# Optimization experiments

Measured on AMD Instinct MI355X. Metric: run time of the kernel, lower is better.

Reference implementation:

```python
import jax, jax.numpy as jnp
import numpy as np

N = 100_000   # nodes
E = 1_280_000 # edges
F_IN = 64
HID = 64

def setup_inputs() -> dict:
    key = jax.random.key(0)
    ks = jax.random.split(key, 5)
    x = jax.random.normal(ks[0], (N, F_IN), dtype=jnp.float32)
    edge_index = jax.random.randint(ks[1], (2, E), 0, N, dtype=jnp.int32)
    edge_weight = jax.random.uniform(ks[2], (E,), dtype=jnp.float32)
    s1 = 1.0 / np.sqrt(F_IN)
    W1 = jax.random.uniform(ks[3], (F_IN, HID), minval=-s1, maxval=s1, dtype=jnp.float32)
    b1 = jnp.zeros((HID,), jnp.float32)
    s2 = 1.0 / np.sqrt(HID)
    W2 = jax.random.uniform(ks[4], (HID, 1), minval=-s2, maxval=s2, dtype=jnp.float32)
    b2 = jnp.zeros((1,), jnp.float32)
    return {"x": x, "edge_index": edge_index, "edge_weight": edge_weight,
            "W1": W1, "b1": b1, "W2": W2, "b2": b2}


def reference(x, edge_index, edge_weight, W1, b1, W2, b2):
    # eval mode: edge dropout and feature dropout are identity.
    # GCNConv with add_self_loops=True: A_hat = A + I, D_hat^-1/2 A_hat D_hat^-1/2.
    row, col = edge_index[0], edge_index[1]
    sl = jnp.arange(N, dtype=row.dtype)
    row = jnp.concatenate([row, sl])
    col = jnp.concatenate([col, sl])
    w = jnp.concatenate([edge_weight, jnp.ones((N,), edge_weight.dtype)])
    # symmetric normalization (shared by both conv layers)
    deg = jax.ops.segment_sum(w, col, num_segments=N)          # [N]
    dinv = jnp.where(deg > 0, jax.lax.rsqrt(deg), 0.0)
    norm = dinv[row] * w * dinv[col]                           # [E+N]

    def gcn(h):  # h: [N, d] already linearly transformed
        msg = h[row] * norm[:, None]                           # gather + scale
        return jax.ops.segment_sum(msg, col, num_segments=N)   # scatter-add

    h = gcn(x @ W1) + b1          # conv1
    h = jax.nn.relu(h)            # relu (dropout = identity in eval)
    out = gcn(h @ W2) + b2        # conv2 -> [N, 1]
    return out
```

## Files before the change

### kernel.cpp

```cpp
#include <hip/hip_runtime.h>
#include <hip/hip_fp16.h>

#define CNT_SHIFT 26
#define DEG_MASK  ((1u << CNT_SHIFT) - 1)
#define DEG_SCALE 1048576.0f
#define CAP 8192
#define GSTRIDE 16

__device__ __forceinline__ unsigned short f_to_h16(float f) {
    return __half_as_ushort(__float2half(f));
}
__device__ __forceinline__ float h16_to_f(unsigned short u) {
    return __half2float(__ushort_as_half(u));
}
__device__ __forceinline__ unsigned long long mkrec(int r, int c, float wv) {
    return (unsigned long long)r | ((unsigned long long)(c & 511) << 17)
         | ((unsigned long long)f_to_h16(wv) << 26);
}

__global__ __launch_bounds__(256) void k_scatter_gemm(
        const int4* __restrict__ row4, const int4* __restrict__ col4, const float4* __restrict__ w4,
        const int* __restrict__ row, const int* __restrict__ col, const float* __restrict__ w,
        unsigned* __restrict__ gcur, unsigned long long* __restrict__ binrec,
        const float* __restrict__ x, const float* __restrict__ W1,
        char* __restrict__ h1q, float* __restrict__ scales,
        int E4, int rem, int nBlkE, int nGemm, int n, int nbkt) {
    __shared__ int h[256];
    __shared__ float xs[4][512];
    int blk = blockIdx.x, t = threadIdx.x;
    if (blk < nBlkE) {
        h[t] = 0;
        __syncthreads();
        int base = blk * 1024;
#pragma unroll
        for (int k = 0; k < 4; ++k) {
            int g = base + k * 256 + t;
            if (g < E4) {
                int4 c = col4[g];
                atomicAdd(&h[c.x >> 9], 1);
                atomicAdd(&h[c.y >> 9], 1);
                atomicAdd(&h[c.z >> 9], 1);
                atomicAdd(&h[c.w >> 9], 1);
            }
        }
        if (blk == 0 && t < rem) atomicAdd(&h[col[4 * E4 + t] >> 9], 1);
        __syncthreads();
        if (t < nbkt) {
            int bb = t + (blk % nbkt);
            bb -= (bb >= nbkt) ? nbkt : 0;
            int cnt = h[bb];
            int runbase = 0;
            if (cnt > 0) runbase = (int)atomicAdd(&gcur[(size_t)bb * GSTRIDE], (unsigned)cnt);
            h[bb] = bb * CAP + runbase;
        }
        __syncthreads();
#pragma unroll
        for (int k = 0; k < 4; ++k) {
            int g = base + k * 256 + t;
            if (g < E4) {
                int4   r = row4[g];
                int4   c = col4[g];
                float4 v = w4[g];
                { int pos = atomicAdd(&h[c.x >> 9], 1); binrec[pos] = mkrec(r.x, c.x, v.x); }
                { int pos = atomicAdd(&h[c.y >> 9], 1); binrec[pos] = mkrec(r.y, c.y, v.y); }
                { int pos = atomicAdd(&h[c.z >> 9], 1); binrec[pos] = mkrec(r.z, c.z, v.z); }
                { int pos = atomicAdd(&h[c.w >> 9], 1); binrec[pos] = mkrec(r.w, c.w, v.w); }
            }
        }
        if (blk == 0 && t < rem) {
            int e = 4 * E4 + t;
            int c = col[e];
            int pos = atomicAdd(&h[c >> 9], 1);
            binrec[pos] = mkrec(row[e], c, w[e]);
        }
    } else {
        int b = blk - nBlkE;
        int lane = t & 63, wave = t >> 6;
        float wr[64];
#pragma unroll
        for (int k = 0; k < 64; ++k) wr[k] = W1[k * 64 + lane];
        const int stride = nGemm * 32;
        for (int base = b * 32 + wave * 8; base < n; base += stride) {
            if (base + 8 <= n) {
                const float4* xsrc = (const float4*)(x + (size_t)base * 64);
                *(float4*)&xs[wave][4 * lane]       = xsrc[lane];
                *(float4*)&xs[wave][256 + 4 * lane] = xsrc[lane + 64];
            } else {
                const float* xf = x + (size_t)base * 64;
                int valid = (n - base) * 64;
                float4 a0, a1;
                int f0 = 4 * lane, f1 = 256 + 4 * lane;
                a0.x = (f0 + 0 < valid) ? xf[f0 + 0] : 0.f;
                a0.y = (f0 + 1 < valid) ? xf[f0 + 1] : 0.f;
                a0.z = (f0 + 2 < valid) ? xf[f0 + 2] : 0.f;
                a0.w = (f0 + 3 < valid) ? xf[f0 + 3] : 0.f;
                a1.x = (f1 + 0 < valid) ? xf[f1 + 0] : 0.f;
                a1.y = (f1 + 1 < valid) ? xf[f1 + 1] : 0.f;
                a1.z = (f1 + 2 < valid) ? xf[f1 + 2] : 0.f;
                a1.w = (f1 + 3 < valid) ? xf[f1 + 3] : 0.f;
                *(float4*)&xs[wave][4 * lane]       = a0;
                *(float4*)&xs[wave][256 + 4 * lane] = a1;
            }
#pragma unroll
            for (int nn = 0; nn < 8; ++nn) {
                int i = base + nn;
                if (i >= n) break;
                float acc = 0.f;
#pragma unroll
                for (int k4 = 0; k4 < 16; ++k4) {
                    float4 xv = *(const float4*)&xs[wave][nn * 64 + 4 * k4];
                    acc = fmaf(xv.x, wr[4 * k4 + 0], acc);
                    acc = fmaf(xv.y, wr[4 * k4 + 1], acc);
                    acc = fmaf(xv.z, wr[4 * k4 + 2], acc);
                    acc = fmaf(xv.w, wr[4 * k4 + 3], acc);
                }
                float m = fabsf(acc);
#pragma unroll
                for (int o = 32; o > 0; o >>= 1) m = fmaxf(m, __shfl_xor(m, o, 64));
                float scale = fmaxf(m, 1e-20f) * (1.0f / 127.0f);
                int q = __float2int_rn(acc / scale);
                h1q[(size_t)i * 64 + lane] = (char)q;
                if (lane == 0) scales[i] = scale;
            }
        }
    }
}

__global__ __launch_bounds__(256) void k_bucket(
        const unsigned long long* __restrict__ binrec, const unsigned* __restrict__ gcur,
        float* __restrict__ dinv, int* __restrict__ off, int* __restrict__ bktend,
        unsigned* __restrict__ ep, float* __restrict__ scales,
        int N, int nbkt) {
    __shared__ unsigned cnt[512];
    __shared__ int   loff[512];
    __shared__ int   ssum[256];
    int b = blockIdx.x, t = threadIdx.x;
    int e0 = b * CAP;
    int tot = (int)gcur[(size_t)b * GSTRIDE];
    int e1 = e0 + tot;
    cnt[t] = 0u; cnt[t + 256] = 0u;
    __syncthreads();
    unsigned epw[32];
    unsigned crk[32];
#pragma unroll
    for (int k = 0; k < 32; ++k) {
        int i = e0 + t + k * 256;
        if (i < e1) {
            unsigned long long rec = binrec[i];
            int cl = (int)((rec >> 17) & 511);
            unsigned hb = (unsigned)((rec >> 26) & 0xFFFF);
            float wv = h16_to_f((unsigned short)hb);
            unsigned old = atomicAdd(&cnt[cl],
                                     (1u << CNT_SHIFT) + (unsigned)(wv * DEG_SCALE + 0.5f));
            unsigned rank = old >> CNT_SHIFT;
            epw[k] = ((unsigned)(rec & 0x1FFFF) << 15) | (hb & 0x7fffu);
            crk[k] = ((unsigned)cl << 16) | rank;
        }
    }
    __syncthreads();
    unsigned p0 = cnt[2 * t], p1 = cnt[2 * t + 1];
    int c0 = (int)(p0 >> CNT_SHIFT), c1 = (int)(p1 >> CNT_SHIFT);
    float d0 = rsqrtf((float)(p0 & DEG_MASK) * (1.0f / DEG_SCALE) + 1.0f);
    float d1 = rsqrtf((float)(p1 & DEG_MASK) * (1.0f / DEG_SCALE) + 1.0f);
    int ps = c0 + c1;
    ssum[t] = ps;
    __syncthreads();
    for (int o = 1; o < 256; o <<= 1) {
        int v = (t >= o) ? ssum[t - o] : 0;
        __syncthreads();
        ssum[t] += v;
        __syncthreads();
    }
    int excl = ssum[t] - ps;
    loff[2 * t] = excl;
    loff[2 * t + 1] = excl + c0;
    int id0 = (b << 9) + 2 * t, id1 = id0 + 1;
    if (id0 < N) { dinv[id0] = d0; scales[id0] *= d0; off[id0] = e0 + excl; }
    if (id1 < N) { dinv[id1] = d1; scales[id1] *= d1; off[id1] = e0 + excl + c0; }
    if (t == 0) bktend[b] = e1;
    __syncthreads();
#pragma unroll
    for (int k = 0; k < 32; ++k) {
        int i = e0 + t + k * 256;
        if (i < e1) {
            int cl   = (int)(crk[k] >> 16);
            int rank = (int)(crk[k] & 0xFFFFu);
            ep[e0 + loff[cl] + rank] = epw[k];
        }
    }
}

__global__ __launch_bounds__(256) void k_agg1(
        const char* __restrict__ h1q, const float* __restrict__ scales,
        const int* __restrict__ off, const int* __restrict__ bktend,
        const unsigned* __restrict__ ep,
        const float* __restrict__ dinv, const float* __restrict__ b1,
        const float* __restrict__ W2,
        float* __restrict__ h2, int n) {
    int lane = threadIdx.x & 63;
    int wave = threadIdx.x >> 6;
    int grp  = lane >> 4;
    int fl   = (lane & 15) * 4;
    int i = blockIdx.x * 4 + wave;
    if (i >= n) return;
    float di = dinv[i];
    float4 acc;
    {
        char4 q4 = *(const char4*)(h1q + (size_t)i * 64 + fl);
        float si = (grp == 0) ? scales[i] : 0.f;
        acc.x = (float)q4.x * si;
        acc.y = (float)q4.y * si;
        acc.z = (float)q4.z * si;
        acc.w = (float)q4.w * si;
    }
    int s = off[i];
    int s1 = (((i & 511) == 511) || (i == n - 1)) ? bktend[i >> 9] : off[i + 1];
    for (; s + 8 <= s1; s += 8) {
        unsigned ea = ep[s + grp];
        unsigned eb = ep[s + 4 + grp];
        const char4 qa = *(const char4*)(h1q + (size_t)(ea >> 15) * 64 + fl);
        const char4 qb = *(const char4*)(h1q + (size_t)(eb >> 15) * 64 + fl);
        float ma = scales[ea >> 15] * h16_to_f((unsigned short)(ea & 0x7fff));
        float mb = scales[eb >> 15] * h16_to_f((unsigned short)(eb & 0x7fff));
        acc.x = fmaf((float)qa.x, ma, acc.x);
        acc.y = fmaf((float)qa.y, ma, acc.y);
        acc.z = fmaf((float)qa.z, ma, acc.z);
        acc.w = fmaf((float)qa.w, ma, acc.w);
        acc.x = fmaf((float)qb.x, mb, acc.x);
        acc.y = fmaf((float)qb.y, mb, acc.y);
        acc.z = fmaf((float)qb.z, mb, acc.z);
        acc.w = fmaf((float)qb.w, mb, acc.w);
    }
    for (; s < s1; s += 4) {
        int idx = s + grp;
        int sI = (idx < s1) ? idx : (s1 - 1);
        unsigned e = ep[sI];
        float m = (idx < s1) ? scales[e >> 15] * h16_to_f((unsigned short)(e & 0x7fff)) : 0.f;
        const char4 q4 = *(const char4*)(h1q + (size_t)(e >> 15) * 64 + fl);
        acc.x = fmaf((float)q4.x, m, acc.x);
        acc.y = fmaf((float)q4.y, m, acc.y);
        acc.z = fmaf((float)q4.z, m, acc.z);
        acc.w = fmaf((float)q4.w, m, acc.w);
    }
    acc.x += __shfl_xor(acc.x, 16, 64); acc.x += __shfl_xor(acc.x, 32, 64);
    acc.y += __shfl_xor(acc.y, 16, 64); acc.y += __shfl_xor(acc.y, 32, 64);
    acc.z += __shfl_xor(acc.z, 16, 64); acc.z += __shfl_xor(acc.z, 32, 64);
    acc.w += __shfl_xor(acc.w, 16, 64); acc.w += __shfl_xor(acc.w, 32, 64);
    float4 bb = *(const float4*)(b1 + fl);
    float4 ww = *(const float4*)(W2 + fl);
    float p = fmaxf(fmaf(di, acc.x, bb.x), 0.f) * ww.x
            + fmaxf(fmaf(di, acc.y, bb.y), 0.f) * ww.y
            + fmaxf(fmaf(di, acc.z, bb.z), 0.f) * ww.z
            + fmaxf(fmaf(di, acc.w, bb.w), 0.f) * ww.w;
#pragma unroll
    for (int o = 1; o < 16; o <<= 1) p += __shfl_xor(p, o, 64);
    if (lane == 0) h2[i] = di * p;
}

__global__ void k_agg2(const float* __restrict__ h2,
                       const int* __restrict__ off, const int* __restrict__ bktend,
                       const unsigned* __restrict__ ep, const float* __restrict__ dinv,
                       const float* __restrict__ b2, float* __restrict__ out, int n) {
    int i = blockIdx.x * 256 + threadIdx.x;
    if (i >= n) return;
    float acc = h2[i];
    int s = off[i];
    int s1 = (((i & 511) == 511) || (i == n - 1)) ? bktend[i >> 9] : off[i + 1];
    for (; s + 8 <= s1; s += 8) {
        unsigned e0 = ep[s],     e1 = ep[s + 1], e2 = ep[s + 2], e3 = ep[s + 3];
        unsigned e4 = ep[s + 4], e5 = ep[s + 5], e6 = ep[s + 6], e7 = ep[s + 7];
        float v0 = h2[e0 >> 15], v1 = h2[e1 >> 15], v2 = h2[e2 >> 15], v3 = h2[e3 >> 15];
        float v4 = h2[e4 >> 15], v5 = h2[e5 >> 15], v6 = h2[e6 >> 15], v7 = h2[e7 >> 15];
        acc = fmaf(v0, h16_to_f((unsigned short)(e0 & 0x7fff)), acc);
        acc = fmaf(v1, h16_to_f((unsigned short)(e1 & 0x7fff)), acc);
        acc = fmaf(v2, h16_to_f((unsigned short)(e2 & 0x7fff)), acc);
        acc = fmaf(v3, h16_to_f((unsigned short)(e3 & 0x7fff)), acc);
        acc = fmaf(v4, h16_to_f((unsigned short)(e4 & 0x7fff)), acc);
        acc = fmaf(v5, h16_to_f((unsigned short)(e5 & 0x7fff)), acc);
        acc = fmaf(v6, h16_to_f((unsigned short)(e6 & 0x7fff)), acc);
        acc = fmaf(v7, h16_to_f((unsigned short)(e7 & 0x7fff)), acc);
    }
    for (; s + 4 <= s1; s += 4) {
        unsigned e0 = ep[s], e1 = ep[s + 1], e2 = ep[s + 2], e3 = ep[s + 3];
        float v0 = h2[e0 >> 15], v1 = h2[e1 >> 15], v2 = h2[e2 >> 15], v3 = h2[e3 >> 15];
        acc = fmaf(v0, h16_to_f((unsigned short)(e0 & 0x7fff)), acc);
        acc = fmaf(v1, h16_to_f((unsigned short)(e1 & 0x7fff)), acc);
        acc = fmaf(v2, h16_to_f((unsigned short)(e2 & 0x7fff)), acc);
        acc = fmaf(v3, h16_to_f((unsigned short)(e3 & 0x7fff)), acc);
    }
    for (; s < s1; ++s) {
        unsigned e = ep[s];
        acc = fmaf(h2[e >> 15], h16_to_f((unsigned short)(e & 0x7fff)), acc);
    }
    out[i] = dinv[i] * acc + b2[0];
}

extern "C" void kernel_launch(void* const* d_in, const int* in_sizes, int n_in,
                              void* d_out, int out_size, void* d_ws, size_t ws_size,
                              hipStream_t stream) {
    const float* x  = (const float*)d_in[0];
    const int*   ei = (const int*)d_in[1];
    const float* w  = (const float*)d_in[2];
    const float* W1 = (const float*)d_in[3];
    const float* b1 = (const float*)d_in[4];
    const float* W2 = (const float*)d_in[5];
    const float* b2 = (const float*)d_in[6];
    float* out = (float*)d_out;

    const int N = in_sizes[0] / 64;
    const int E = in_sizes[2];
    const int* row = ei;
    const int* col = ei + E;

    const int nbkt  = (N + 511) >> 9;
    const int E4    = E / 4;
    const int rem   = E - 4 * E4;
    const int nBlkE = (E4 + 1023) / 1024;
    const int nGemm = 1024;

    char* p = (char*)d_ws;
    auto take = [&](size_t bytes) { char* q = p; p += (bytes + 15) & ~(size_t)15; return q; };
    unsigned long long* binrec = (unsigned long long*)take((size_t)nbkt * CAP * 8);
    unsigned* gcur = (unsigned*)take((size_t)nbkt * GSTRIDE * 4);
    int* bktend  = (int*)take((size_t)nbkt * 4);
    char* h1q    = (char*)take((size_t)N * 64);
    float* scales= (float*)take((size_t)N * 4);
    float* dinv  = (float*)take((size_t)N * 4);
    int*   off   = (int*)take((size_t)(N + 1) * 4);
    unsigned* ep = (unsigned*)take((size_t)nbkt * CAP * 4);
    float* h2    = (float*)take((size_t)N * 4);

    (void)hipMemsetAsync(gcur, 0, (size_t)nbkt * GSTRIDE * 4, stream);
    k_scatter_gemm<<<nBlkE + nGemm, 256, 0, stream>>>(
        (const int4*)row, (const int4*)col, (const float4*)w,
        row, col, w, gcur, binrec, x, W1, h1q, scales,
        E4, rem, nBlkE, nGemm, N, nbkt);
    k_bucket<<<nbkt, 256, 0, stream>>>(binrec, gcur, dinv, off, bktend, ep, scales, N, nbkt);
    k_agg1<<<(N + 3) / 4, 256, 0, stream>>>(h1q, scales, off, bktend, ep, dinv, b1, W2, h2, N);
    k_agg2<<<(N + 255) / 256, 256, 0, stream>>>(h2, off, bktend, ep, dinv, b2, out, N);
}
```

Baseline: 194.3 us.

## Compute x@W1 with bf16 MFMA 16x16x32 instead of scalar FMA

Replaces the per-lane scalar FP32 dot-product GEMM (x staged in LDS, W1 column held in registers) with bf16 MFMA instructions on 16-row tiles. x is loaded straight from global memory and converted to bf16, W1 is preloaded into B fragments, and the int8 quantization with per-row max reduction is redone on the MFMA output layout. The aim is to cut ALU time in the GEMM blocks that run alongside edge binning. The cost is reduced precision from bf16 inputs, on top of the existing int8 quantization of h1, and byte stores with a 16-element stride.

```diff
diff --git a/kernel.cpp b/kernel.cpp
--- a/kernel.cpp
+++ b/kernel.cpp
@@ -7,11 +7,19 @@
 #define CAP 8192
 #define GSTRIDE 16
 
+typedef __attribute__((ext_vector_type(8))) short short8;
+typedef __attribute__((ext_vector_type(4))) float v4f;
+
 __device__ __forceinline__ unsigned short f_to_h16(float f) {
     return __half_as_ushort(__float2half(f));
 }
 __device__ __forceinline__ float h16_to_f(unsigned short u) {
     return __half2float(__ushort_as_half(u));
+}
+__device__ __forceinline__ unsigned short f_to_bf16(float f) {
+    unsigned int u = __float_as_uint(f);
+    u += 0x7fffu + ((u >> 16) & 1u);
+    return (unsigned short)(u >> 16);
 }
 __device__ __forceinline__ unsigned long long mkrec(int r, int c, float wv) {
     return (unsigned long long)r | ((unsigned long long)(c & 511) << 17)
@@ -26,7 +34,6 @@
         char* __restrict__ h1q, float* __restrict__ scales,
         int E4, int rem, int nBlkE, int nGemm, int n, int nbkt) {
     __shared__ int h[256];
-    __shared__ float xs[4][512];
     int blk = blockIdx.x, t = threadIdx.x;
     if (blk < nBlkE) {
         h[t] = 0;
@@ -75,52 +82,77 @@
         }
     } else {
         int b = blk - nBlkE;
-        int lane = t & 63, wave = t >> 6;
-        float wr[64];
-#pragma unroll
-        for (int k = 0; k < 64; ++k) wr[k] = W1[k * 64 + lane];
-        const int stride = nGemm * 32;
-        for (int base = b * 32 + wave * 8; base < n; base += stride) {
-            if (base + 8 <= n) {
-                const float4* xsrc = (const float4*)(x + (size_t)base * 64);
-                *(float4*)&xs[wave][4 * lane]       = xsrc[lane];
-                *(float4*)&xs[wave][256 + 4 * lane] = xsrc[lane + 64];
+        int lane = t & 63;
+        int wave = t >> 6;
+        int q   = lane >> 4;
+        int n16 = lane & 15;
+        short8 bf[8];
+#pragma unroll
+        for (int ct = 0; ct < 4; ++ct) {
+#pragma unroll
+            for (int hh = 0; hh < 2; ++hh) {
+                short8 v;
+#pragma unroll
+                for (int j = 0; j < 8; ++j)
+                    v[j] = (short)f_to_bf16(W1[(hh * 32 + q * 8 + j) * 64 + ct * 16 + n16]);
+                bf[ct * 2 + hh] = v;
+            }
+        }
+        int ntile = (n + 15) >> 4;
+        int stride = nGemm * 4;
+        for (int tile = b * 4 + wave; tile < ntile; tile += stride) {
+            int base = tile << 4;
+            short8 a0, a1;
+            if (base + 16 <= n) {
+                const float* xr = x + (size_t)(base + n16) * 64 + q * 8;
+                float4 u0 = *(const float4*)(xr);
+                float4 u1 = *(const float4*)(xr + 4);
+                float4 u2 = *(const float4*)(xr + 32);
+                float4 u3 = *(const float4*)(xr + 36);
+                a0[0] = (short)f_to_bf16(u0.x); a0[1] = (short)f_to_bf16(u0.y);
+                a0[2] = (short)f_to_bf16(u0.z); a0[3] = (short)f_to_bf16(u0.w);
+                a0[4] = (short)f_to_bf16(u1.x); a0[5] = (short)f_to_bf16(u1.y);
+                a0[6] = (short)f_to_bf16(u1.z); a0[7] = (short)f_to_bf16(u1.w);
+                a1[0] = (short)f_to_bf16(u2.x); a1[1] = (short)f_to_bf16(u2.y);
+                a1[2] = (short)f_to_bf16(u2.z); a1[3] = (short)f_to_bf16(u2.w);
+                a1[4] = (short)f_to_bf16(u3.x); a1[5] = (short)f_to_bf16(u3.y);
+                a1[6] = (short)f_to_bf16(u3.z); a1[7] = (short)f_to_bf16(u3.w);
             } else {
-                const float* xf = x + (size_t)base * 64;
-                int valid = (n - base) * 64;
-                float4 a0, a1;
-                int f0 = 4 * lane, f1 = 256 + 4 * lane;
-                a0.x = (f0 + 0 < valid) ? xf[f0 + 0] : 0.f;
-                a0.y = (f0 + 1 < valid) ? xf[f0 + 1] : 0.f;
-                a0.z = (f0 + 2 < valid) ? xf[f0 + 2] : 0.f;
-                a0.w = (f0 + 3 < valid) ? xf[f0 + 3] : 0.f;
-                a1.x = (f1 + 0 < valid) ? xf[f1 + 0] : 0.f;
-                a1.y = (f1 + 1 < valid) ? xf[f1 + 1] : 0.f;
-                a1.z = (f1 + 2 < valid) ? xf[f1 + 2] : 0.f;
-                a1.w = (f1 + 3 < valid) ? xf[f1 + 3] : 0.f;
-                *(float4*)&xs[wave][4 * lane]       = a0;
-                *(float4*)&xs[wave][256 + 4 * lane] = a1;
-            }
-#pragma unroll
-            for (int nn = 0; nn < 8; ++nn) {
-                int i = base + nn;
-                if (i >= n) break;
-                float acc = 0.f;
-#pragma unroll
-                for (int k4 = 0; k4 < 16; ++k4) {
-                    float4 xv = *(const float4*)&xs[wave][nn * 64 + 4 * k4];
-                    acc = fmaf(xv.x, wr[4 * k4 + 0], acc);
-                    acc = fmaf(xv.y, wr[4 * k4 + 1], acc);
-                    acc = fmaf(xv.z, wr[4 * k4 + 2], acc);
-                    acc = fmaf(xv.w, wr[4 * k4 + 3], acc);
+                bool ok = (base + n16) < n;
+                const float* xr = x + (size_t)(ok ? (base + n16) : 0) * 64 + q * 8;
+#pragma unroll
+                for (int j = 0; j < 8; ++j) {
+                    a0[j] = ok ? (short)f_to_bf16(xr[j])      : (short)0;
+                    a1[j] = ok ? (short)f_to_bf16(xr[32 + j]) : (short)0;
                 }
-                float m = fabsf(acc);
-#pragma unroll
-                for (int o = 32; o > 0; o >>= 1) m = fmaxf(m, __shfl_xor(m, o, 64));
-                float scale = fmaxf(m, 1e-20f) * (1.0f / 127.0f);
-                int q = __float2int_rn(acc / scale);
-                h1q[(size_t)i * 64 + lane] = (char)q;
-                if (lane == 0) scales[i] = scale;
+            }
+            v4f acc0 = {0.f, 0.f, 0.f, 0.f}, acc1 = acc0, acc2 = acc0, acc3 = acc0;
+            acc0 = __builtin_amdgcn_mfma_f32_16x16x32_bf16(a0, bf[0], acc0, 0, 0, 0);
+            acc0 = __builtin_amdgcn_mfma_f32_16x16x32_bf16(a1, bf[1], acc0, 0, 0, 0);
+            acc1 = __builtin_amdgcn_mfma_f32_16x16x32_bf16(a0, bf[2], acc1, 0, 0, 0);
+            acc1 = __builtin_amdgcn_mfma_f32_16x16x32_bf16(a1, bf[3], acc1, 0, 0, 0);
+            acc2 = __builtin_amdgcn_mfma_f32_16x16x32_bf16(a0, bf[4], acc2, 0, 0, 0);
+            acc2 = __builtin_amdgcn_mfma_f32_16x16x32_bf16(a1, bf[5], acc2, 0, 0, 0);
+            acc3 = __builtin_amdgcn_mfma_f32_16x16x32_bf16(a0, bf[6], acc3, 0, 0, 0);
+            acc3 = __builtin_amdgcn_mfma_f32_16x16x32_bf16(a1, bf[7], acc3, 0, 0, 0);
+#pragma unroll
+            for (int r = 0; r < 4; ++r) {
+                int rowg = base + q * 4 + r;
+                if (rowg >= n) break;
+                float m = fmaxf(fmaxf(fabsf(acc0[r]), fabsf(acc1[r])),
+                                fmaxf(fabsf(acc2[r]), fabsf(acc3[r])));
+                m = fmaxf(m, __shfl_xor(m, 1, 64));
+                m = fmaxf(m, __shfl_xor(m, 2, 64));
+                m = fmaxf(m, __shfl_xor(m, 4, 64));
+                m = fmaxf(m, __shfl_xor(m, 8, 64));
+                m = fmaxf(m, 1e-20f);
+                float inv = 127.0f / m;
+                char* dst = h1q + (size_t)rowg * 64 + n16;
+                dst[0]  = (char)__float2int_rn(acc0[r] * inv);
+                dst[16] = (char)__float2int_rn(acc1[r] * inv);
+                dst[32] = (char)__float2int_rn(acc2[r] * inv);
+                dst[48] = (char)__float2int_rn(acc3[r] * inv);
+                if (n16 == 0) scales[rowg] = m * (1.0f / 127.0f);
             }
         }
     }
```

Result: faster. 181.9 us (-6.4%).
